# Kernel tuning notes

Measured on AMD Instinct MI355X. Metric: run time of the kernel, lower is better.

The kernel has to match this reference:

```python
import jax, jax.numpy as jnp
import numpy as np

NUM_EXPERTS = 8
TOP_K = 2
ENTROPY_WEIGHT = 0.1
MAX_USAGE_RATIO = 0.3


def setup_inputs() -> dict:
    key = jax.random.key(0)
    k0, k1, k2 = jax.random.split(key, 3)
    B, S, D, H, E = 4, 4096, 1024, 1024, NUM_EXPERTS
    x = jax.random.normal(k0, (B, S, D), jnp.float32)
    gate_w = jax.random.normal(k1, (D, E), jnp.float32) * (1.0 / np.sqrt(D))
    gate_b = jnp.zeros((E,), jnp.float32)
    expert_w = jax.random.normal(k2, (E, D, H), jnp.float32) * (1.0 / np.sqrt(D))
    expert_b = jnp.zeros((E, H), jnp.float32)
    return {"x": x, "gate_w": gate_w, "gate_b": gate_b,
            "expert_w": expert_w, "expert_b": expert_b}


def reference(x, gate_w, gate_b, expert_w, expert_b):
    # x: [B, S, D]; dropout omitted (eval mode / deterministic reference)
    B, S, D = x.shape
    E = gate_w.shape[1]
    H = expert_w.shape[2]
    N = B * S
    xf = x.reshape(N, D)

    gate_logits = xf @ gate_w + gate_b            # [N, E]
    gate_probs = jax.nn.softmax(gate_logits, axis=-1)
    entropy = -jnp.sum(gate_probs * jnp.log(gate_probs + 1e-10), axis=-1).mean()
    entropy_loss = ENTROPY_WEIGHT * entropy

    topk_probs, topk_idx = jax.lax.top_k(gate_probs, TOP_K)   # [N, K]
    onehot = jax.nn.one_hot(topk_idx, E, dtype=xf.dtype)       # [N, K, E]
    combine = jnp.einsum('nk,nke->ne', topk_probs, onehot)     # [N, E] gating weight per expert

    # Weighted combine of per-expert Linear outputs; loop over small fixed E.
    out = jnp.zeros((N, H), xf.dtype)
    for e in range(E):
        out = out + combine[:, e:e + 1] * (xf @ expert_w[e] + expert_b[e])

    counts = jnp.sum(onehot, axis=(0, 1))                      # [E] tokens routed per expert
    usage_ratios = counts / N
    overuse_penalty = jnp.sum(jax.nn.relu(usage_ratios - MAX_USAGE_RATIO))

    return out.reshape(B, S, H), entropy_loss + overuse_penalty
```

## Files before the change

### kernel.cpp

```cpp
#include <hip/hip_runtime.h>
#include <hip/hip_bf16.h>

typedef __bf16 bf16x8 __attribute__((ext_vector_type(8)));
typedef __bf16 bf16x4 __attribute__((ext_vector_type(4)));
typedef float  f32x4  __attribute__((ext_vector_type(4)));

#define NTOK 16384
#define DDIM 1024
#define HDIM 1024
#define CNT_STRIDE 16

#define XB_OFF   0u
#define WT_OFF   33554432u
#define IDXP_OFF 50331648u
#define PPP_OFF  50397184u
#define TPID_OFF 50528256u
#define TPP_OFF  50593792u
#define CNT_OFF  50724864u
#define CUR_OFF  50728960u
#define BASE_OFF 50733056u
#define TILT_OFF 50733312u
#define NT_OFF   50736384u
#define ENT_OFF  50736388u
#define ZERO_LEN 11536u

typedef __attribute__((address_space(1))) void gvoid_t;
typedef __attribute__((address_space(3))) void lvoid_t;

__device__ __forceinline__ void cp16(void* lds, const void* g) {
  __builtin_amdgcn_global_load_lds((gvoid_t*)g, (lvoid_t*)lds, 16, 0, 0);
}

__global__ __launch_bounds__(256) void transpose_w(const float* __restrict__ w,
                                                   __bf16* __restrict__ wT) {
  const int b  = blockIdx.x;
  const int e  = b >> 8;
  const int d0 = ((b >> 4) & 15) * 64;
  const int h0 = (b & 15) * 64;
  __shared__ float tile[64][68];
  const int t = threadIdx.x;
  const float* base = w + ((size_t)e * DDIM + d0) * HDIM + h0;
#pragma unroll
  for (int it = 0; it < 4; ++it) {
    int dl = it * 16 + (t >> 4);
    int hl = (t & 15) * 4;
    float4 v = *(const float4*)(base + (size_t)dl * HDIM + hl);
    tile[dl][hl]     = v.x;
    tile[dl][hl + 1] = v.y;
    tile[dl][hl + 2] = v.z;
    tile[dl][hl + 3] = v.w;
  }
  __syncthreads();
  __bf16* obase = wT + ((size_t)e * HDIM + h0) * DDIM + d0;
#pragma unroll
  for (int it = 0; it < 4; ++it) {
    int hl = it * 16 + (t >> 4);
    int dl = (t & 15) * 4;
    bf16x4 bv;
    bv[0] = (__bf16)tile[dl][hl];
    bv[1] = (__bf16)tile[dl + 1][hl];
    bv[2] = (__bf16)tile[dl + 2][hl];
    bv[3] = (__bf16)tile[dl + 3][hl];
    *(bf16x4*)(obase + (size_t)hl * DDIM + dl) = bv;
  }
}

__global__ __launch_bounds__(256) void gate_kernel(
    const float* __restrict__ x, const float* __restrict__ gw,
    const float* __restrict__ gb, __bf16* __restrict__ xb,
    int* __restrict__ tt_pid, float2* __restrict__ tt_pp,
    int* __restrict__ cnt_g, float* __restrict__ ent_g) {
  __shared__ float gwT[8 * 1024];
  __shared__ int   lcnt[64];
  __shared__ float went[4];
  const int tid = threadIdx.x, w = tid >> 6, lane = tid & 63;
  for (int i = tid; i < 64; i += 256) lcnt[i] = 0;
#pragma unroll
  for (int i = 0; i < 32; ++i) {
    int lin = i * 256 + tid;
    gwT[(lin & 7) * 1024 + (lin >> 3)] = gw[lin];
  }
  __syncthreads();
  float4 gr[4][8];
#pragma unroll
  for (int j = 0; j < 4; ++j)
#pragma unroll
    for (int e = 0; e < 8; ++e)
      gr[j][e] = *(const float4*)&gwT[e * 1024 + j * 256 + lane * 4];
  float gbr[8];
#pragma unroll
  for (int e = 0; e < 8; ++e) gbr[e] = gb[e];

  float entacc = 0.f;
  for (int t = 0; t < 4; ++t) {
    const int n = blockIdx.x * 16 + w * 4 + t;
    float acc[8] = {0.f, 0.f, 0.f, 0.f, 0.f, 0.f, 0.f, 0.f};
#pragma unroll
    for (int j = 0; j < 4; ++j) {
      float4 v = *(const float4*)(x + (size_t)n * DDIM + j * 256 + lane * 4);
      bf16x4 bv;
      bv[0] = (__bf16)v.x; bv[1] = (__bf16)v.y;
      bv[2] = (__bf16)v.z; bv[3] = (__bf16)v.w;
      *(bf16x4*)(xb + (size_t)n * DDIM + j * 256 + lane * 4) = bv;
#pragma unroll
      for (int e = 0; e < 8; ++e) {
        float4 g = gr[j][e];
        acc[e] += v.x * g.x + v.y * g.y + v.z * g.z + v.w * g.w;
      }
    }
#pragma unroll
    for (int e = 0; e < 8; ++e) {
      float s = acc[e];
#pragma unroll
      for (int off = 1; off < 64; off <<= 1) s += __shfl_xor(s, off);
      acc[e] = s;
    }
    float p[8];
    float mx = -1e30f;
#pragma unroll
    for (int e = 0; e < 8; ++e) { p[e] = acc[e] + gbr[e]; mx = fmaxf(mx, p[e]); }
    float s = 0.f;
#pragma unroll
    for (int e = 0; e < 8; ++e) { p[e] = expf(p[e] - mx); s += p[e]; }
    float inv = 1.0f / s;
    float ent = 0.f;
#pragma unroll
    for (int e = 0; e < 8; ++e) { p[e] *= inv; ent -= p[e] * logf(p[e] + 1e-10f); }
    entacc += ent;
    int e1 = 0; float p1 = p[0];
#pragma unroll
    for (int e = 1; e < 8; ++e) if (p[e] > p1) { p1 = p[e]; e1 = e; }
    int e2 = (e1 == 0) ? 1 : 0; float p2 = p[e2];
#pragma unroll
    for (int e = 0; e < 8; ++e) if (e != e1 && p[e] > p2) { p2 = p[e]; e2 = e; }
    int   elo = (e1 < e2) ? e1 : e2;
    int   ehi = (e1 < e2) ? e2 : e1;
    float plo = (e1 < e2) ? p1 : p2;
    float phi = (e1 < e2) ? p2 : p1;
    int pid = elo * 8 + ehi;
    if (lane == 0) {
      tt_pid[n] = pid;
      tt_pp[n]  = make_float2(plo, phi);
      atomicAdd(&lcnt[pid], 1);
    }
  }
  if (lane == 0) went[w] = entacc;
  __syncthreads();
  if (tid < 64 && lcnt[tid]) atomicAdd(&cnt_g[tid * CNT_STRIDE], lcnt[tid]);
  if (tid == 0)
    atomicAdd(ent_g, went[0] + went[1] + went[2] + went[3]);
}

__global__ void scan_kernel(const int* __restrict__ cnt_g, int* __restrict__ base_g,
                            int4* __restrict__ tilt, int* __restrict__ nt_g,
                            const float* __restrict__ ent_g, float* __restrict__ loss_out) {
  if (threadIdx.x == 0) {
    int b = 0, t = 0;
    int ecnt[8] = {0, 0, 0, 0, 0, 0, 0, 0};
    for (int pid = 0; pid < 64; ++pid) {
      int c = cnt_g[pid * CNT_STRIDE];
      base_g[pid] = b;
      if (c > 0) {
        ecnt[pid >> 3] += c;
        ecnt[pid & 7]  += c;
        for (int r = 0; r < c; r += 128) tilt[t++] = make_int4(pid, r, c, b);
        b += c;
      }
    }
    *nt_g = t;
    float pen = 0.f;
    for (int e = 0; e < 8; ++e) {
      float r = (float)ecnt[e] / (float)NTOK - 0.3f;
      if (r > 0.f) pen += r;
    }
    loss_out[0] = 0.1f * (ent_g[0] / (float)NTOK) + pen;
  }
}

__global__ __launch_bounds__(256) void scatter_kernel(
    const int* __restrict__ tt_pid, const float2* __restrict__ tt_pp,
    const int* __restrict__ base_g, int* __restrict__ cur_g,
    int* __restrict__ idx_p, float2* __restrict__ pp_p) {
  __shared__ int lcnt[64], lbase[64];
  const int tid = threadIdx.x;
  if (tid < 64) lcnt[tid] = 0;
  __syncthreads();
  const int n = blockIdx.x * 256 + tid;
  const int pid = tt_pid[n];
  int lofs = atomicAdd(&lcnt[pid], 1);
  __syncthreads();
  if (tid < 64 && lcnt[tid]) lbase[tid] = atomicAdd(&cur_g[tid * CNT_STRIDE], lcnt[tid]);
  __syncthreads();
  int dst = base_g[pid] + lbase[pid] + lofs;
  idx_p[dst] = n;
  pp_p[dst]  = tt_pp[n];
}

__global__ __launch_bounds__(256) void moe_gemm(
    const __bf16* __restrict__ xb, const __bf16* __restrict__ wT,
    const float* __restrict__ eb, const int* __restrict__ idx_p,
    const float2* __restrict__ pp_p, const int4* __restrict__ tilt,
    const int* __restrict__ nt_g, float* __restrict__ out) {
  const int gy = blockIdx.y;
  if (gy >= *nt_g) return;
  const int4 te = tilt[gy];
  const int pid = te.x, row0 = te.y, cntp = te.z, gbase = te.w;
  const int elo = pid >> 3, ehi = pid & 7;
  const int gx = blockIdx.x;

  __shared__ __bf16 Ash[128 * 64];
  __shared__ __bf16 BloS[128 * 64];
  __shared__ __bf16 BhiS[128 * 64];
  __shared__ int    tok_s[128];
  __shared__ float2 pp_s[128];

  const int tid = threadIdx.x, w = tid >> 6, lane = tid & 63;
  if (tid < 128) {
    int s = row0 + tid;
    int g = gbase + ((s < cntp) ? s : (cntp - 1));
    tok_s[tid] = idx_p[g];
    pp_s[tid]  = pp_p[g];
  }
  __syncthreads();

  f32x4 accL[4][4], accH[4][4];
  const f32x4 zero = {0.f, 0.f, 0.f, 0.f};
#pragma unroll
  for (int mi = 0; mi < 4; ++mi)
#pragma unroll
    for (int ni = 0; ni < 4; ++ni) { accL[mi][ni] = zero; accH[mi][ni] = zero; }

  const int wm = (w >> 1) * 64, wn = (w & 1) * 64;
  const int tq = lane >> 4, tr = lane & 15, tr7 = tr & 7;
  const int rsub = lane >> 3;
  const int csw = ((lane & 7) ^ rsub) * 8;

  const __bf16* wlo = wT + (size_t)elo * HDIM * DDIM + (size_t)(gx * 128) * DDIM;
  const __bf16* whi = wT + (size_t)ehi * HDIM * DDIM + (size_t)(gx * 128) * DDIM;
  const __bf16* aptr[4];
  const __bf16* lptr[4];
  const __bf16* hptr[4];
#pragma unroll
  for (int it = 0; it < 4; ++it) {
    int r = it * 32 + w * 8 + rsub;
    aptr[it] = xb + (size_t)tok_s[r] * DDIM + csw;
    lptr[it] = wlo + (size_t)r * DDIM + csw;
    hptr[it] = whi + (size_t)r * DDIM + csw;
  }

  for (int kk = 0; kk < 16; ++kk) {
#pragma unroll
    for (int it = 0; it < 4; ++it) {
      const int rb = it * 32 + w * 8;
      cp16((char*)Ash  + rb * 128, aptr[it]); aptr[it] += 64;
      cp16((char*)BloS + rb * 128, lptr[it]); lptr[it] += 64;
      cp16((char*)BhiS + rb * 128, hptr[it]); hptr[it] += 64;
    }
    __syncthreads();
#pragma unroll
    for (int h = 0; h < 2; ++h) {
      const int co = (h << 2) | tq;
      bf16x8 a[4], bl[4], bh[4];
#pragma unroll
      for (int mi = 0; mi < 4; ++mi)
        a[mi] = *(const bf16x8*)((const char*)Ash + (wm + mi * 16 + tr) * 128 +
                                 ((co ^ tr7) << 4));
#pragma unroll
      for (int ni = 0; ni < 4; ++ni) {
        bl[ni] = *(const bf16x8*)((const char*)BloS + (wn + ni * 16 + tr) * 128 +
                                  ((co ^ tr7) << 4));
        bh[ni] = *(const bf16x8*)((const char*)BhiS + (wn + ni * 16 + tr) * 128 +
                                  ((co ^ tr7) << 4));
      }
#pragma unroll
      for (int mi = 0; mi < 4; ++mi)
#pragma unroll
        for (int ni = 0; ni < 4; ++ni) {
          accL[mi][ni] = __builtin_amdgcn_mfma_f32_16x16x32_bf16(a[mi], bl[ni], accL[mi][ni], 0, 0, 0);
          accH[mi][ni] = __builtin_amdgcn_mfma_f32_16x16x32_bf16(a[mi], bh[ni], accH[mi][ni], 0, 0, 0);
        }
    }
    __syncthreads();
  }

  float blov[4], bhiv[4];
#pragma unroll
  for (int ni = 0; ni < 4; ++ni) {
    int col = gx * 128 + wn + ni * 16 + tr;
    blov[ni] = eb[elo * HDIM + col];
    bhiv[ni] = eb[ehi * HDIM + col];
  }
#pragma unroll
  for (int mi = 0; mi < 4; ++mi)
#pragma unroll
    for (int r = 0; r < 4; ++r) {
      int lr = wm + mi * 16 + tq * 4 + r;
      if (row0 + lr < cntp) {
        int    tok = tok_s[lr];
        float2 pp  = pp_s[lr];
        float* orow = out + (size_t)tok * HDIM + gx * 128 + wn + tr;
#pragma unroll
        for (int ni = 0; ni < 4; ++ni)
          orow[ni * 16] = pp.x * (accL[mi][ni][r] + blov[ni]) +
                          pp.y * (accH[mi][ni][r] + bhiv[ni]);
      }
    }
}

extern "C" void kernel_launch(void* const* d_in, const int* in_sizes, int n_in,
                              void* d_out, int out_size, void* d_ws, size_t ws_size,
                              hipStream_t stream) {
  const float* x  = (const float*)d_in[0];
  const float* gw = (const float*)d_in[1];
  const float* gb = (const float*)d_in[2];
  const float* ew = (const float*)d_in[3];
  const float* eb = (const float*)d_in[4];
  float* out = (float*)d_out;
  char*  ws  = (char*)d_ws;

  __bf16* xb     = (__bf16*)(ws + XB_OFF);
  __bf16* wT     = (__bf16*)(ws + WT_OFF);
  int*    idx_p  = (int*)(ws + IDXP_OFF);
  float2* pp_p   = (float2*)(ws + PPP_OFF);
  int*    tt_pid = (int*)(ws + TPID_OFF);
  float2* tt_pp  = (float2*)(ws + TPP_OFF);
  int*    cnt_g  = (int*)(ws + CNT_OFF);
  int*    cur_g  = (int*)(ws + CUR_OFF);
  int*    base_g = (int*)(ws + BASE_OFF);
  int4*   tilt   = (int4*)(ws + TILT_OFF);
  int*    nt_g   = (int*)(ws + NT_OFF);
  float*  ent_g  = (float*)(ws + ENT_OFF);

  hipMemsetAsync(ws + CNT_OFF, 0, ZERO_LEN, stream);
  transpose_w<<<dim3(2048), 256, 0, stream>>>(ew, wT);
  gate_kernel<<<dim3(1024), 256, 0, stream>>>(x, gw, gb, xb, tt_pid, tt_pp,
                                              cnt_g, ent_g);
  scan_kernel<<<1, 64, 0, stream>>>(cnt_g, base_g, tilt, nt_g, ent_g,
                                    out + (size_t)NTOK * HDIM);
  scatter_kernel<<<dim3(64), 256, 0, stream>>>(tt_pid, tt_pp, base_g, cur_g,
                                               idx_p, pp_p);
  moe_gemm<<<dim3(8, 160), 256, 0, stream>>>(xb, wT, eb, idx_p, pp_p, tilt,
                                             nt_g, out);
}
```

Baseline: 335.5 us.

## Prefetch GEMM tiles into registers, overlap global loads with MFMA compute

The grouped expert GEMM now loads the next K-slice of A and both weight tiles into registers while the current slice is used for MFMA compute. It stores them to LDS with regular swizzled writes in place of direct global-to-LDS loads, with custom barriers that only wait on LDS counters. Separately, the entropy is computed as log(sum) minus the probability-weighted logits, which needs one log per token instead of eight. The scan kernel also stages the counts in shared memory. The register prefetch adds VGPR pressure and can lower occupancy.

```diff
diff --git a/kernel.cpp b/kernel.cpp
--- a/kernel.cpp
+++ b/kernel.cpp
@@ -24,12 +24,12 @@
 #define ENT_OFF  50736388u
 #define ZERO_LEN 11536u
 
-typedef __attribute__((address_space(1))) void gvoid_t;
-typedef __attribute__((address_space(3))) void lvoid_t;
-
-__device__ __forceinline__ void cp16(void* lds, const void* g) {
-  __builtin_amdgcn_global_load_lds((gvoid_t*)g, (lvoid_t*)lds, 16, 0, 0);
-}
+#define BAR()                                                    \
+  do {                                                           \
+    asm volatile("s_waitcnt lgkmcnt(0)" ::: "memory");           \
+    __builtin_amdgcn_s_barrier();                                \
+    asm volatile("" ::: "memory");                               \
+  } while (0)
 
 __global__ __launch_bounds__(256) void transpose_w(const float* __restrict__ w,
                                                    __bf16* __restrict__ wT) {
@@ -115,18 +115,18 @@
       for (int off = 1; off < 64; off <<= 1) s += __shfl_xor(s, off);
       acc[e] = s;
     }
-    float p[8];
+    float p[8], lg[8];
     float mx = -1e30f;
 #pragma unroll
     for (int e = 0; e < 8; ++e) { p[e] = acc[e] + gbr[e]; mx = fmaxf(mx, p[e]); }
     float s = 0.f;
 #pragma unroll
-    for (int e = 0; e < 8; ++e) { p[e] = expf(p[e] - mx); s += p[e]; }
+    for (int e = 0; e < 8; ++e) { lg[e] = p[e] - mx; p[e] = expf(lg[e]); s += p[e]; }
     float inv = 1.0f / s;
-    float ent = 0.f;
-#pragma unroll
-    for (int e = 0; e < 8; ++e) { p[e] *= inv; ent -= p[e] * logf(p[e] + 1e-10f); }
-    entacc += ent;
+    float dot = 0.f;
+#pragma unroll
+    for (int e = 0; e < 8; ++e) { p[e] *= inv; dot += p[e] * lg[e]; }
+    entacc += logf(s) - dot;
     int e1 = 0; float p1 = p[0];
 #pragma unroll
     for (int e = 1; e < 8; ++e) if (p[e] > p1) { p1 = p[e]; e1 = e; }
@@ -154,20 +154,24 @@
 __global__ void scan_kernel(const int* __restrict__ cnt_g, int* __restrict__ base_g,
                             int4* __restrict__ tilt, int* __restrict__ nt_g,
                             const float* __restrict__ ent_g, float* __restrict__ loss_out) {
-  if (threadIdx.x == 0) {
-    int b = 0, t = 0;
+  __shared__ int csh[64];
+  const int t = threadIdx.x;
+  csh[t] = cnt_g[t * CNT_STRIDE];
+  __syncthreads();
+  if (t == 0) {
+    int b = 0, ti = 0;
     int ecnt[8] = {0, 0, 0, 0, 0, 0, 0, 0};
     for (int pid = 0; pid < 64; ++pid) {
-      int c = cnt_g[pid * CNT_STRIDE];
+      int c = csh[pid];
       base_g[pid] = b;
       if (c > 0) {
         ecnt[pid >> 3] += c;
         ecnt[pid & 7]  += c;
-        for (int r = 0; r < c; r += 128) tilt[t++] = make_int4(pid, r, c, b);
+        for (int r = 0; r < c; r += 128) tilt[ti++] = make_int4(pid, r, c, b);
         b += c;
       }
     }
-    *nt_g = t;
+    *nt_g = ti;
     float pen = 0.f;
     for (int e = 0; e < 8; ++e) {
       float r = (float)ecnt[e] / (float)NTOK - 0.3f;
@@ -233,30 +237,50 @@
   const int wm = (w >> 1) * 64, wn = (w & 1) * 64;
   const int tq = lane >> 4, tr = lane & 15, tr7 = tr & 7;
   const int rsub = lane >> 3;
-  const int csw = ((lane & 7) ^ rsub) * 8;
+  const int cg   = lane & 7;
+  const int csw  = cg ^ rsub;
 
   const __bf16* wlo = wT + (size_t)elo * HDIM * DDIM + (size_t)(gx * 128) * DDIM;
   const __bf16* whi = wT + (size_t)ehi * HDIM * DDIM + (size_t)(gx * 128) * DDIM;
   const __bf16* aptr[4];
   const __bf16* lptr[4];
   const __bf16* hptr[4];
+  int wofs[4];
 #pragma unroll
   for (int it = 0; it < 4; ++it) {
     int r = it * 32 + w * 8 + rsub;
-    aptr[it] = xb + (size_t)tok_s[r] * DDIM + csw;
-    lptr[it] = wlo + (size_t)r * DDIM + csw;
-    hptr[it] = whi + (size_t)r * DDIM + csw;
+    aptr[it] = xb + (size_t)tok_s[r] * DDIM + cg * 8;
+    lptr[it] = wlo + (size_t)r * DDIM + cg * 8;
+    hptr[it] = whi + (size_t)r * DDIM + cg * 8;
+    wofs[it] = r * 128 + csw * 16;
+  }
+
+  bf16x8 ra[4], rl[4], rh[4];
+#pragma unroll
+  for (int it = 0; it < 4; ++it) {
+    ra[it] = *(const bf16x8*)aptr[it]; aptr[it] += 64;
+    rl[it] = *(const bf16x8*)lptr[it]; lptr[it] += 64;
+    rh[it] = *(const bf16x8*)hptr[it]; hptr[it] += 64;
   }
 
   for (int kk = 0; kk < 16; ++kk) {
 #pragma unroll
     for (int it = 0; it < 4; ++it) {
-      const int rb = it * 32 + w * 8;
-      cp16((char*)Ash  + rb * 128, aptr[it]); aptr[it] += 64;
-      cp16((char*)BloS + rb * 128, lptr[it]); lptr[it] += 64;
-      cp16((char*)BhiS + rb * 128, hptr[it]); hptr[it] += 64;
-    }
-    __syncthreads();
+      *(bf16x8*)((char*)Ash  + wofs[it]) = ra[it];
+      *(bf16x8*)((char*)BloS + wofs[it]) = rl[it];
+      *(bf16x8*)((char*)BhiS + wofs[it]) = rh[it];
+    }
+    BAR();
+
+    if (kk < 15) {
+#pragma unroll
+      for (int it = 0; it < 4; ++it) {
+        ra[it] = *(const bf16x8*)aptr[it]; aptr[it] += 64;
+        rl[it] = *(const bf16x8*)lptr[it]; lptr[it] += 64;
+        rh[it] = *(const bf16x8*)hptr[it]; hptr[it] += 64;
+      }
+    }
+
 #pragma unroll
     for (int h = 0; h < 2; ++h) {
       const int co = (h << 2) | tq;
@@ -280,7 +304,7 @@
           accH[mi][ni] = __builtin_amdgcn_mfma_f32_16x16x32_bf16(a[mi], bh[ni], accH[mi][ni], 0, 0, 0);
         }
     }
-    __syncthreads();
+    BAR();
   }
 
   float blov[4], bhiv[4];
```

Result: faster. 326.8 us (-2.6%).

## Double-buffer MoE GEMM LDS tiles and tidy transpose, entropy, scan

Applied to the files above, without the earlier changes.

The grouped expert GEMM now uses two LDS buffers per operand. The next K-slice is prefetched with global_load_lds while MFMAs run on the current slice, and one barrier per iteration is removed. The weight transpose writes 8-wide bf16 vectors and pads the tile differently to cut LDS bank conflicts. The gate entropy is computed as log(sum) minus dot(p, logit), dropping eight logs per token, and the scan kernel stages counts through shared memory. Doubling LDS to about 96KB per block may reduce occupancy. The prefetch also relies on the single barrier to order the async copy into the buffer being overwritten.

```diff
diff --git a/kernel.cpp b/kernel.cpp
--- a/kernel.cpp
+++ b/kernel.cpp
@@ -37,7 +37,7 @@
   const int e  = b >> 8;
   const int d0 = ((b >> 4) & 15) * 64;
   const int h0 = (b & 15) * 64;
-  __shared__ float tile[64][68];
+  __shared__ float tile[64][69];
   const int t = threadIdx.x;
   const float* base = w + ((size_t)e * DDIM + d0) * HDIM + h0;
 #pragma unroll
@@ -53,15 +53,13 @@
   __syncthreads();
   __bf16* obase = wT + ((size_t)e * HDIM + h0) * DDIM + d0;
 #pragma unroll
-  for (int it = 0; it < 4; ++it) {
-    int hl = it * 16 + (t >> 4);
-    int dl = (t & 15) * 4;
-    bf16x4 bv;
-    bv[0] = (__bf16)tile[dl][hl];
-    bv[1] = (__bf16)tile[dl + 1][hl];
-    bv[2] = (__bf16)tile[dl + 2][hl];
-    bv[3] = (__bf16)tile[dl + 3][hl];
-    *(bf16x4*)(obase + (size_t)hl * DDIM + dl) = bv;
+  for (int it = 0; it < 2; ++it) {
+    int hl = it * 32 + (t >> 3);
+    int dl = (t & 7) * 8;
+    bf16x8 bv;
+#pragma unroll
+    for (int i = 0; i < 8; ++i) bv[i] = (__bf16)tile[dl + i][hl];
+    *(bf16x8*)(obase + (size_t)hl * DDIM + dl) = bv;
   }
 }
 
@@ -115,18 +113,18 @@
       for (int off = 1; off < 64; off <<= 1) s += __shfl_xor(s, off);
       acc[e] = s;
     }
-    float p[8];
+    float p[8], lg[8];
     float mx = -1e30f;
 #pragma unroll
     for (int e = 0; e < 8; ++e) { p[e] = acc[e] + gbr[e]; mx = fmaxf(mx, p[e]); }
     float s = 0.f;
 #pragma unroll
-    for (int e = 0; e < 8; ++e) { p[e] = expf(p[e] - mx); s += p[e]; }
+    for (int e = 0; e < 8; ++e) { lg[e] = p[e] - mx; p[e] = expf(lg[e]); s += p[e]; }
     float inv = 1.0f / s;
-    float ent = 0.f;
-#pragma unroll
-    for (int e = 0; e < 8; ++e) { p[e] *= inv; ent -= p[e] * logf(p[e] + 1e-10f); }
-    entacc += ent;
+    float dot = 0.f;
+#pragma unroll
+    for (int e = 0; e < 8; ++e) { p[e] *= inv; dot += p[e] * lg[e]; }
+    entacc += logf(s) - dot;
     int e1 = 0; float p1 = p[0];
 #pragma unroll
     for (int e = 1; e < 8; ++e) if (p[e] > p1) { p1 = p[e]; e1 = e; }
@@ -154,20 +152,24 @@
 __global__ void scan_kernel(const int* __restrict__ cnt_g, int* __restrict__ base_g,
                             int4* __restrict__ tilt, int* __restrict__ nt_g,
                             const float* __restrict__ ent_g, float* __restrict__ loss_out) {
-  if (threadIdx.x == 0) {
-    int b = 0, t = 0;
+  __shared__ int csh[64];
+  const int t = threadIdx.x;
+  csh[t] = cnt_g[t * CNT_STRIDE];
+  __syncthreads();
+  if (t == 0) {
+    int b = 0, ti = 0;
     int ecnt[8] = {0, 0, 0, 0, 0, 0, 0, 0};
     for (int pid = 0; pid < 64; ++pid) {
-      int c = cnt_g[pid * CNT_STRIDE];
+      int c = csh[pid];
       base_g[pid] = b;
       if (c > 0) {
         ecnt[pid >> 3] += c;
         ecnt[pid & 7]  += c;
-        for (int r = 0; r < c; r += 128) tilt[t++] = make_int4(pid, r, c, b);
+        for (int r = 0; r < c; r += 128) tilt[ti++] = make_int4(pid, r, c, b);
         b += c;
       }
     }
-    *nt_g = t;
+    *nt_g = ti;
     float pen = 0.f;
     for (int e = 0; e < 8; ++e) {
       float r = (float)ecnt[e] / (float)NTOK - 0.3f;
@@ -208,9 +210,9 @@
   const int elo = pid >> 3, ehi = pid & 7;
   const int gx = blockIdx.x;
 
-  __shared__ __bf16 Ash[128 * 64];
-  __shared__ __bf16 BloS[128 * 64];
-  __shared__ __bf16 BhiS[128 * 64];
+  __shared__ __bf16 Ash [2][128 * 64];
+  __shared__ __bf16 BloS[2][128 * 64];
+  __shared__ __bf16 BhiS[2][128 * 64];
   __shared__ int    tok_s[128];
   __shared__ float2 pp_s[128];
 
@@ -248,28 +250,40 @@
     hptr[it] = whi + (size_t)r * DDIM + csw;
   }
 
+#pragma unroll
+  for (int it = 0; it < 4; ++it) {
+    const int rb = it * 32 + w * 8;
+    cp16((char*)Ash[0]  + rb * 128, aptr[it]); aptr[it] += 64;
+    cp16((char*)BloS[0] + rb * 128, lptr[it]); lptr[it] += 64;
+    cp16((char*)BhiS[0] + rb * 128, hptr[it]); hptr[it] += 64;
+  }
+  __syncthreads();
+
+  int cur = 0;
   for (int kk = 0; kk < 16; ++kk) {
-#pragma unroll
-    for (int it = 0; it < 4; ++it) {
-      const int rb = it * 32 + w * 8;
-      cp16((char*)Ash  + rb * 128, aptr[it]); aptr[it] += 64;
-      cp16((char*)BloS + rb * 128, lptr[it]); lptr[it] += 64;
-      cp16((char*)BhiS + rb * 128, hptr[it]); hptr[it] += 64;
-    }
-    __syncthreads();
+    if (kk < 15) {
+#pragma unroll
+      for (int it = 0; it < 4; ++it) {
+        const int rb = it * 32 + w * 8;
+        cp16((char*)Ash[cur ^ 1]  + rb * 128, aptr[it]); aptr[it] += 64;
+        cp16((char*)BloS[cur ^ 1] + rb * 128, lptr[it]); lptr[it] += 64;
+        cp16((char*)BhiS[cur ^ 1] + rb * 128, hptr[it]); hptr[it] += 64;
+      }
+    }
+
 #pragma unroll
     for (int h = 0; h < 2; ++h) {
       const int co = (h << 2) | tq;
       bf16x8 a[4], bl[4], bh[4];
 #pragma unroll
       for (int mi = 0; mi < 4; ++mi)
-        a[mi] = *(const bf16x8*)((const char*)Ash + (wm + mi * 16 + tr) * 128 +
+        a[mi] = *(const bf16x8*)((const char*)Ash[cur] + (wm + mi * 16 + tr) * 128 +
                                  ((co ^ tr7) << 4));
 #pragma unroll
       for (int ni = 0; ni < 4; ++ni) {
-        bl[ni] = *(const bf16x8*)((const char*)BloS + (wn + ni * 16 + tr) * 128 +
+        bl[ni] = *(const bf16x8*)((const char*)BloS[cur] + (wn + ni * 16 + tr) * 128 +
                                   ((co ^ tr7) << 4));
-        bh[ni] = *(const bf16x8*)((const char*)BhiS + (wn + ni * 16 + tr) * 128 +
+        bh[ni] = *(const bf16x8*)((const char*)BhiS[cur] + (wn + ni * 16 + tr) * 128 +
                                   ((co ^ tr7) << 4));
       }
 #pragma unroll
@@ -280,7 +294,8 @@
           accH[mi][ni] = __builtin_amdgcn_mfma_f32_16x16x32_bf16(a[mi], bh[ni], accH[mi][ni], 0, 0, 0);
         }
     }
-    __syncthreads();
+
+    if (kk < 15) { __syncthreads(); cur ^= 1; }
   }
 
   float blov[4], bhiv[4];
```

After: 341.8 us. No clear change (+1.9%).
